# Optimization experiments

Hardware: AMD Instinct MI355X
Metric: run time of the kernel (lower is better)

Reference implementation:

```python
import jax, jax.numpy as jnp
import numpy as np

SCALE = float(np.sqrt(512.0))  # NOTE: module MULTIPLIES by sqrt(dim_attn), not divides


def setup_inputs() -> dict:
    key = jax.random.key(0)
    ks = jax.random.split(key, 10)
    B, N, DQ, DKV, DA = 4, 2048, 512, 512, 512
    w = 0.02  # small init so the *sqrt(d) score scaling stays numerically sane
    return {
        "query": jax.random.normal(ks[0], (B, N, DQ), jnp.float32),
        "key_value": jax.random.normal(ks[1], (B, N, DKV), jnp.float32),
        "Wq": jax.random.normal(ks[2], (DQ, DA), jnp.float32) * w,
        "bq": jnp.zeros((DA,), jnp.float32),
        "Wk": jax.random.normal(ks[3], (DKV, DA), jnp.float32) * w,
        "bk": jnp.zeros((DA,), jnp.float32),
        "Wv": jax.random.normal(ks[4], (DKV, DA), jnp.float32) * w,
        "bv": jnp.zeros((DA,), jnp.float32),
        "Wo": jax.random.normal(ks[5], (DA, DQ), jnp.float32) * w,
        "bo": jnp.zeros((DQ,), jnp.float32),
    }


def reference(query, key_value, Wq, bq, Wk, bk, Wv, bv, Wo, bo):
    # q/k/v projections: (..., dim) @ (dim, dim_attn)
    q = query @ Wq + bq          # [b, nq, da]
    k = key_value @ Wk + bk      # [b, nk, da]
    v = key_value @ Wv + bv      # [b, nk, da]
    # einsum 'dac,dbc->dab' then *sqrt(dim_attn) (faithful: multiply, not divide)
    attn = jnp.einsum('bqc,bkc->bqk', q, k) * SCALE
    attn = jax.nn.softmax(attn, axis=-1)
    # dropout p=0.0 -> no-op
    out = jnp.einsum('bqk,bkc->bqc', attn, v)
    return query + (out @ Wo + bo)
```

## Files before the change

kernel.cpp:

```cpp
#include <hip/hip_runtime.h>

typedef unsigned short u16;
typedef unsigned int u32;
typedef __attribute__((ext_vector_type(8))) __bf16 bf16x8;
typedef __attribute__((ext_vector_type(4))) float f32x4;

#define BK 32

__device__ __forceinline__ u16 f2bf(float x) {
    u32 u = __float_as_uint(x);
    u = (u + 0x7FFFu + ((u >> 16) & 1u)) >> 16;
    return (u16)u;
}
__device__ __forceinline__ float bf2f(u16 h) { return __uint_as_float(((u32)h) << 16); }

#define GLD16(g, l)                                                                        \
    __builtin_amdgcn_global_load_lds((const __attribute__((address_space(1))) void*)(g),   \
                                     (__attribute__((address_space(3))) void*)(l), 16, 0, 0)

template <int N>
__device__ __forceinline__ void vm_wait() {
    if constexpr (N == 0) asm volatile("s_waitcnt vmcnt(0)" ::: "memory");
    else if constexpr (N == 1) asm volatile("s_waitcnt vmcnt(1)" ::: "memory");
    else if constexpr (N == 2) asm volatile("s_waitcnt vmcnt(2)" ::: "memory");
    else if constexpr (N == 3) asm volatile("s_waitcnt vmcnt(3)" ::: "memory");
    else if constexpr (N == 4) asm volatile("s_waitcnt vmcnt(4)" ::: "memory");
    else if constexpr (N == 6) asm volatile("s_waitcnt vmcnt(6)" ::: "memory");
    else if constexpr (N == 8) asm volatile("s_waitcnt vmcnt(8)" ::: "memory");
    else static_assert(N == 0, "unsupported vmcnt literal");
}
#define SBAR() asm volatile("s_barrier" ::: "memory")

__global__ __launch_bounds__(256) void prep_k(
    const float* __restrict__ q, const float* __restrict__ kv,
    u16* __restrict__ QXh, u16* __restrict__ QXl,
    u16* __restrict__ KVh, u16* __restrict__ KVl, long nblk, long n4,
    const float* __restrict__ Wq, const float* __restrict__ Wk,
    const float* __restrict__ Wv, const float* __restrict__ Wo,
    u16* __restrict__ WqTh, u16* __restrict__ WqTl,
    u16* __restrict__ WkvTh, u16* __restrict__ WkvTl,
    u16* __restrict__ WoTh, u16* __restrict__ WoTl, int dim) {
    long b = blockIdx.x;
    if (b < 2 * nblk) {
        const float* x = q; u16* h = QXh; u16* l = QXl;
        if (b >= nblk) { b -= nblk; x = kv; h = KVh; l = KVl; }
        long i = b * 256 + threadIdx.x;
        if (i >= n4) return;
        float4 v = ((const float4*)x)[i];
        float xs[4] = {v.x, v.y, v.z, v.w};
        u16 hh[4], ll[4];
#pragma unroll
        for (int qq = 0; qq < 4; ++qq) {
            hh[qq] = f2bf(xs[qq]);
            ll[qq] = f2bf(xs[qq] - bf2f(hh[qq]));
        }
        uint2 ph, pl;
        ph.x = hh[0] | ((u32)hh[1] << 16); ph.y = hh[2] | ((u32)hh[3] << 16);
        pl.x = ll[0] | ((u32)ll[1] << 16); pl.y = ll[2] | ((u32)ll[3] << 16);
        ((uint2*)h)[i] = ph;
        ((uint2*)l)[i] = pl;
        return;
    }
    long tb = b - 2 * nblk;
    const int z = (int)(tb >> 8);
    const int rem = (int)(tb & 255);
    const long DD = (long)dim * dim;
    const float* W; u16* Th; u16* Tl;
    switch (z) {
        case 0: W = Wq; Th = WqTh; Tl = WqTl; break;
        case 1: W = Wk; Th = WkvTh; Tl = WkvTl; break;
        case 2: W = Wv; Th = WkvTh + DD; Tl = WkvTl + DD; break;
        default: W = Wo; Th = WoTh; Tl = WoTl; break;
    }
    __shared__ float tile[32][33];
    const int bx = (rem & 15) * 32;
    const int by = (rem >> 4) * 32;
    const int tx = threadIdx.x & 31, ty = threadIdx.x >> 5;
    for (int i = 0; i < 32; i += 8)
        tile[ty + i][tx] = W[(size_t)(by + ty + i) * dim + bx + tx];
    __syncthreads();
    for (int i = 0; i < 32; i += 8) {
        float x = tile[tx][ty + i];
        u16 h = f2bf(x);
        size_t idx = (size_t)(bx + ty + i) * dim + by + tx;
        Th[idx] = h;
        Tl[idx] = f2bf(x - bf2f(h));
    }
}

__global__ __launch_bounds__(256) void softmax_k(float* __restrict__ S, int N) {
    float* row = S + (size_t)blockIdx.x * N;
    const int t = threadIdx.x;
    float4 va = ((const float4*)row)[2 * t];
    float4 vb = ((const float4*)row)[2 * t + 1];
    float v[8] = {va.x, va.y, va.z, va.w, vb.x, vb.y, vb.z, vb.w};
    float m = v[0];
#pragma unroll
    for (int i = 1; i < 8; i++) m = fmaxf(m, v[i]);
#pragma unroll
    for (int o = 32; o; o >>= 1) m = fmaxf(m, __shfl_xor(m, o));
    __shared__ float smax[4], ssum[4];
    if ((t & 63) == 0) smax[t >> 6] = m;
    __syncthreads();
    m = fmaxf(fmaxf(smax[0], smax[1]), fmaxf(smax[2], smax[3]));
    float s = 0.f;
#pragma unroll
    for (int i = 0; i < 8; i++) { v[i] = __expf(v[i] - m); s += v[i]; }
#pragma unroll
    for (int o = 32; o; o >>= 1) s += __shfl_xor(s, o);
    if ((t & 63) == 0) ssum[t >> 6] = s;
    __syncthreads();
    s = ssum[0] + ssum[1] + ssum[2] + ssum[3];
    const float inv = 1.0f / s;
    u32 w0 = f2bf(v[0] * inv) | ((u32)f2bf(v[1] * inv) << 16);
    u32 w1 = f2bf(v[2] * inv) | ((u32)f2bf(v[3] * inv) << 16);
    u32 w2 = f2bf(v[4] * inv) | ((u32)f2bf(v[5] * inv) << 16);
    u32 w3 = f2bf(v[6] * inv) | ((u32)f2bf(v[7] * inv) << 16);
    uint4 o4; o4.x = w0; o4.y = w1; o4.z = w2; o4.w = w3;
    ((uint4*)row)[t] = o4;
}

struct GemmArgs {
    const u16 *Ah, *Al; long lda, strideA;
    const u16 *BTh, *BTl; long ldb, strideBT;
    const float *bias1, *bias2; int nsplit;
    const float* resid; long ldres; float scale;
    float* Cf; long ldcf;
    u16 *Cbh, *Cbl; long ldcb;
    u16* CbT; long tRows, tChans, ldct;
    long strideC; int K;
};

template <int SPLIT, int BMt, int BNt>
struct SmemT {
    u16 AsH[2][BMt * BK];
    u16 BsH[2][BNt * BK];
    u16 AsL[2][(SPLIT ? BMt : 1) * BK];
    u16 BsL[2][(SPLIT ? BNt : 1) * BK];
};

template <int SPLIT, int BMt, int BNt, int WR, int WC>
__device__ __forceinline__ void gemm_body(SmemT<SPLIT, BMt, BNt>& sm, const GemmArgs& g,
                                          int bxi, int byi, long bz) {
    static_assert(WR * WC == 4, "4 waves");
    constexpr int MI = BMt / WR / 16;
    constexpr int NJ = BNt / WC / 16;
    constexpr int PA = BMt / 64;
    constexpr int PB = BNt / 64;
    constexpr int NLD = (PA + PB) * (SPLIT ? 2 : 1);

    const u16* Ah = g.Ah + bz * g.strideA;
    const u16* BTh = g.BTh + bz * g.strideBT;
    const u16* Al = nullptr; const u16* BTl = nullptr;
    if constexpr (SPLIT) { Al = g.Al + bz * g.strideA; BTl = g.BTl + bz * g.strideBT; }
    float* Cf = g.Cf ? g.Cf + bz * g.strideC : nullptr;
    u16* Cbh = g.Cbh ? g.Cbh + bz * g.strideC : nullptr;
    u16* Cbl = g.Cbl ? g.Cbl + bz * g.strideC : nullptr;

    const int t = threadIdx.x;
    const int w = t >> 6, lane = t & 63;
    const int l15 = lane & 15, quad = lane >> 4;
    const int m0 = bxi * BMt, n0 = byi * BNt;
    const int wrow = (w / WC) * (BMt / WR);
    const int wcol = (w % WC) * (BNt / WC);

    const u16* gAh[PA]; const u16* gAl[PA]; int lA[PA];
    const u16* gBh[PB]; const u16* gBl[PB]; int lB[PB];
#pragma unroll
    for (int p = 0; p < PA; ++p) {
        int slot = p * 256 + t;
        int r = slot >> 2, c = slot & 3;
        int cg = c ^ ((r >> 1) & 3);
        gAh[p] = Ah + (long)(m0 + r) * g.lda + cg * 8;
        if constexpr (SPLIT) gAl[p] = Al + (long)(m0 + r) * g.lda + cg * 8;
        lA[p] = (p * 256 + w * 64) * 8;
    }
#pragma unroll
    for (int p = 0; p < PB; ++p) {
        int slot = p * 256 + t;
        int r = slot >> 2, c = slot & 3;
        int cg = c ^ ((r >> 1) & 3);
        gBh[p] = BTh + (long)(n0 + r) * g.ldb + cg * 8;
        if constexpr (SPLIT) gBl[p] = BTl + (long)(n0 + r) * g.ldb + cg * 8;
        lB[p] = (p * 256 + w * 64) * 8;
    }

    int aoff[MI], boff[NJ];
#pragma unroll
    for (int i = 0; i < MI; ++i) {
        int r = wrow + i * 16 + l15;
        aoff[i] = (r * 4 + (quad ^ ((r >> 1) & 3))) * 8;
    }
#pragma unroll
    for (int j = 0; j < NJ; ++j) {
        int r = wcol + j * 16 + l15;
        boff[j] = (r * 4 + (quad ^ ((r >> 1) & 3))) * 8;
    }

    f32x4 acc[MI][NJ];
#pragma unroll
    for (int i = 0; i < MI; i++)
#pragma unroll
        for (int j = 0; j < NJ; j++) acc[i][j] = (f32x4){0.f, 0.f, 0.f, 0.f};

    auto stage = [&](int buf) {
#pragma unroll
        for (int p = 0; p < PA; ++p) {
            GLD16(gAh[p], &sm.AsH[buf][lA[p]]);
            gAh[p] += BK;
            if constexpr (SPLIT) { GLD16(gAl[p], &sm.AsL[buf][lA[p]]); gAl[p] += BK; }
        }
#pragma unroll
        for (int p = 0; p < PB; ++p) {
            GLD16(gBh[p], &sm.BsH[buf][lB[p]]);
            gBh[p] += BK;
            if constexpr (SPLIT) { GLD16(gBl[p], &sm.BsL[buf][lB[p]]); gBl[p] += BK; }
        }
    };

    auto compute = [&](int buf) {
        bf16x8 aH[MI], bH[NJ];
#pragma unroll
        for (int i = 0; i < MI; ++i) aH[i] = *(const bf16x8*)&sm.AsH[buf][aoff[i]];
#pragma unroll
        for (int j = 0; j < NJ; ++j) bH[j] = *(const bf16x8*)&sm.BsH[buf][boff[j]];
        if constexpr (SPLIT) {
            bf16x8 aL[MI], bL[NJ];
#pragma unroll
            for (int i = 0; i < MI; ++i) aL[i] = *(const bf16x8*)&sm.AsL[buf][aoff[i]];
#pragma unroll
            for (int j = 0; j < NJ; ++j) bL[j] = *(const bf16x8*)&sm.BsL[buf][boff[j]];
#pragma unroll
            for (int i = 0; i < MI; ++i)
#pragma unroll
                for (int j = 0; j < NJ; ++j) {
                    acc[i][j] = __builtin_amdgcn_mfma_f32_16x16x32_bf16(aH[i], bH[j], acc[i][j], 0, 0, 0);
                    acc[i][j] = __builtin_amdgcn_mfma_f32_16x16x32_bf16(aH[i], bL[j], acc[i][j], 0, 0, 0);
                    acc[i][j] = __builtin_amdgcn_mfma_f32_16x16x32_bf16(aL[i], bH[j], acc[i][j], 0, 0, 0);
                }
        } else {
#pragma unroll
            for (int i = 0; i < MI; ++i)
#pragma unroll
                for (int j = 0; j < NJ; ++j)
                    acc[i][j] = __builtin_amdgcn_mfma_f32_16x16x32_bf16(aH[i], bH[j], acc[i][j], 0, 0, 0);
        }
    };

    const int nt = g.K / BK;
    stage(0);
    if (nt > 1) stage(1);
    for (int tt = 0; tt < nt; tt += 2) {
        if (tt + 1 < nt) vm_wait<NLD>(); else vm_wait<0>();
        SBAR();
        compute(0);
        SBAR();
        if (tt + 2 < nt) stage(0);
        if (tt + 1 < nt) {
            if (tt + 2 < nt) vm_wait<NLD>(); else vm_wait<0>();
            SBAR();
            compute(1);
            SBAR();
            if (tt + 3 < nt) stage(1);
        }
    }

#pragma unroll
    for (int i = 0; i < MI; ++i) {
#pragma unroll
        for (int j = 0; j < NJ; ++j) {
            const int mBase = m0 + wrow + i * 16 + quad * 4;
            const int nn = n0 + wcol + j * 16 + l15;
            const bool norm = nn < g.nsplit;
            float bvs;
            if (norm) bvs = g.bias1 ? g.bias1[nn] : 0.f;
            else bvs = g.bias2 ? g.bias2[nn - g.nsplit] : 0.f;
#pragma unroll
            for (int r = 0; r < 4; ++r) {
                const long row = mBase + r;
                float x = acc[i][j][r] * g.scale + bvs;
                if (g.resid) x += g.resid[row * g.ldres + nn];
                if (norm) {
                    if (Cf) Cf[row * g.ldcf + nn] = x;
                    if (Cbh) {
                        u16 h = f2bf(x);
                        Cbh[row * g.ldcb + nn] = h;
                        if (Cbl) Cbl[row * g.ldcb + nn] = f2bf(x - bf2f(h));
                    }
                } else {
                    long b = row / g.tRows, qq = row - b * g.tRows;
                    g.CbT[(b * g.tChans + (nn - g.nsplit)) * g.ldct + qq] = f2bf(x);
                }
            }
        }
    }
}

template <int SPLIT, int BMt, int BNt, int WR, int WC>
__global__ __launch_bounds__(256) void gemm_k(GemmArgs g) {
    __shared__ SmemT<SPLIT, BMt, BNt> sm;
    gemm_body<SPLIT, BMt, BNt, WR, WC>(sm, g, blockIdx.x, blockIdx.y, blockIdx.z);
}

template <int SPLIT, int BMt, int BNt, int WR, int WC>
__global__ __launch_bounds__(256) void gemm2_k(GemmArgs g0, int ny0, GemmArgs g1) {
    __shared__ SmemT<SPLIT, BMt, BNt> sm;
    if ((int)blockIdx.y < ny0)
        gemm_body<SPLIT, BMt, BNt, WR, WC>(sm, g0, blockIdx.x, blockIdx.y, blockIdx.z);
    else
        gemm_body<SPLIT, BMt, BNt, WR, WC>(sm, g1, blockIdx.x, blockIdx.y - ny0, blockIdx.z);
}

extern "C" void kernel_launch(void* const* d_in, const int* in_sizes, int n_in,
                              void* d_out, int out_size, void* d_ws, size_t ws_size,
                              hipStream_t stream) {
    const float* query = (const float*)d_in[0];
    const float* kv    = (const float*)d_in[1];
    const float* Wq = (const float*)d_in[2];
    const float* bq = (const float*)d_in[3];
    const float* Wk = (const float*)d_in[4];
    const float* bk = (const float*)d_in[5];
    const float* Wv = (const float*)d_in[6];
    const float* bv = (const float*)d_in[7];
    const float* Wo = (const float*)d_in[8];
    const float* bo = (const float*)d_in[9];
    float* out = (float*)d_out;

    const int B = 4, N = 2048, D = 512;
    const long MD = (long)B * N * D;
    const int BIG = 1 << 30;

    char* p = (char*)d_ws;
    auto alloc = [&](size_t bytes) { void* r = (void*)p; p += (bytes + 255) & ~(size_t)255; return r; };
    float* S = (float*)alloc((long)B * N * N * 4);
    u16* QXh = (u16*)S;
    u16* QXl = QXh + MD;
    u16* KVh = QXl + MD;
    u16* KVl = KVh + MD;
    u16* Qh = (u16*)alloc(MD * 2);
    u16* Ql = (u16*)alloc(MD * 2);
    u16* Kh = (u16*)alloc(MD * 2);
    u16* Kl = (u16*)alloc(MD * 2);
    u16* Vt = (u16*)alloc(MD * 2);
    u16* Oh = (u16*)alloc(MD * 2);
    u16* WqTh = (u16*)alloc((long)D * D * 2);
    u16* WqTl = (u16*)alloc((long)D * D * 2);
    u16* WkvTh = (u16*)alloc((long)2 * D * D * 2);
    u16* WkvTl = (u16*)alloc((long)2 * D * D * 2);
    u16* WoTh = (u16*)alloc((long)D * D * 2);
    u16* WoTl = (u16*)alloc((long)D * D * 2);

    const dim3 blk(256, 1, 1);
    const float SCALE = 22.627416997969522f;

    prep_k<<<dim3(2 * 4096 + 1024, 1, 1), blk, 0, stream>>>(
        query, kv, QXh, QXl, KVh, KVl, 4096, MD / 4,
        Wq, Wk, Wv, Wo, WqTh, WqTl, WkvTh, WkvTl, WoTh, WoTl, D);

    GemmArgs qa{};
    qa.Ah = QXh; qa.Al = QXl; qa.lda = D; qa.strideA = 0;
    qa.BTh = WqTh; qa.BTl = WqTl; qa.ldb = D; qa.strideBT = 0;
    qa.bias1 = bq; qa.bias2 = nullptr; qa.nsplit = BIG;
    qa.resid = nullptr; qa.ldres = 0; qa.scale = 1.0f;
    qa.Cf = nullptr; qa.ldcf = 0;
    qa.Cbh = Qh; qa.Cbl = Ql; qa.ldcb = D;
    qa.CbT = nullptr; qa.tRows = 1; qa.tChans = 1; qa.ldct = 1;
    qa.strideC = 0; qa.K = D;

    GemmArgs ka{};
    ka.Ah = KVh; ka.Al = KVl; ka.lda = D; ka.strideA = 0;
    ka.BTh = WkvTh; ka.BTl = WkvTl; ka.ldb = D; ka.strideBT = 0;
    ka.bias1 = bk; ka.bias2 = bv; ka.nsplit = D;
    ka.resid = nullptr; ka.ldres = 0; ka.scale = 1.0f;
    ka.Cf = nullptr; ka.ldcf = 0;
    ka.Cbh = Kh; ka.Cbl = Kl; ka.ldcb = D;
    ka.CbT = Vt; ka.tRows = N; ka.tChans = D; ka.ldct = N;
    ka.strideC = 0; ka.K = D;
    gemm2_k<1, 128, 64, 2, 2><<<dim3(64, 24, 1), blk, 0, stream>>>(qa, 8, ka);

    GemmArgs sa{};
    sa.Ah = Qh; sa.Al = Ql; sa.lda = D; sa.strideA = (long)N * D;
    sa.BTh = Kh; sa.BTl = Kl; sa.ldb = D; sa.strideBT = (long)N * D;
    sa.bias1 = nullptr; sa.bias2 = nullptr; sa.nsplit = BIG;
    sa.resid = nullptr; sa.ldres = 0; sa.scale = SCALE;
    sa.Cf = S; sa.ldcf = N;
    sa.Cbh = nullptr; sa.Cbl = nullptr; sa.ldcb = 0;
    sa.CbT = nullptr; sa.tRows = 1; sa.tChans = 1; sa.ldct = 1;
    sa.strideC = (long)N * N; sa.K = D;
    gemm_k<1, 128, 64, 2, 2><<<dim3(16, 32, 4), blk, 0, stream>>>(sa);

    softmax_k<<<dim3(B * N, 1, 1), blk, 0, stream>>>(S, N);

    GemmArgs pa{};
    pa.Ah = (const u16*)S; pa.Al = nullptr; pa.lda = 2L * N; pa.strideA = (long)N * 2 * N;
    pa.BTh = Vt; pa.BTl = nullptr; pa.ldb = N; pa.strideBT = (long)D * N;
    pa.bias1 = nullptr; pa.bias2 = nullptr; pa.nsplit = BIG;
    pa.resid = nullptr; pa.ldres = 0; pa.scale = 1.0f;
    pa.Cf = nullptr; pa.ldcf = 0;
    pa.Cbh = Oh; pa.Cbl = nullptr; pa.ldcb = D;
    pa.CbT = nullptr; pa.tRows = 1; pa.tChans = 1; pa.ldct = 1;
    pa.strideC = (long)N * D; pa.K = N;
    gemm_k<0, 128, 64, 2, 2><<<dim3(16, 8, 4), blk, 0, stream>>>(pa);

    GemmArgs oa{};
    oa.Ah = Oh; oa.Al = nullptr; oa.lda = D; oa.strideA = 0;
    oa.BTh = WoTh; oa.BTl = nullptr; oa.ldb = D; oa.strideBT = 0;
    oa.bias1 = bo; oa.bias2 = nullptr; oa.nsplit = BIG;
    oa.resid = query; oa.ldres = D; oa.scale = 1.0f;
    oa.Cf = out; oa.ldcf = D;
    oa.Cbh = nullptr; oa.Cbl = nullptr; oa.ldcb = 0;
    oa.CbT = nullptr; oa.tRows = 1; oa.tChans = 1; oa.ldct = 1;
    oa.strideC = 0; oa.K = D;
    gemm_k<0, 128, 64, 2, 2><<<dim3(64, 8, 1), blk, 0, stream>>>(oa);

    (void)in_sizes; (void)n_in; (void)out_size; (void)ws_size;
}
```

Before: 330.4 us.

## Use 8-wave GEMM blocks with per-wave A/B staging split

Switches all GEMM kernels from 4 to 8 waves per 128x64 tile (4x2 wave grid), halving each wave's accumulator footprint. Global-to-LDS staging is reorganised so every wave loads one 16-byte chunk of A, and only the first four waves load B. Per-wave vmcnt waits are adjusted to the differing load counts. The aim is more latency hiding and more MFMA issue parallelism per CU, at the cost of fewer MFMAs per LDS read and more barrier participants.

Result: faster. 279.8 us (-15.3%).

```diff
diff --git a/kernel.cpp b/kernel.cpp
--- a/kernel.cpp
+++ b/kernel.cpp
@@ -142,12 +142,15 @@
 template <int SPLIT, int BMt, int BNt, int WR, int WC>
 __device__ __forceinline__ void gemm_body(SmemT<SPLIT, BMt, BNt>& sm, const GemmArgs& g,
                                           int bxi, int byi, long bz) {
-    static_assert(WR * WC == 4, "4 waves");
+    constexpr int WAVES = WR * WC;
+    static_assert(WAVES == 8, "8-wave kernel");
+    static_assert(BMt / 16 == WAVES, "A staging = 1 GLD16 per wave");
+    constexpr int BW = BNt / 16;
+    static_assert(BW <= WAVES, "");
     constexpr int MI = BMt / WR / 16;
     constexpr int NJ = BNt / WC / 16;
-    constexpr int PA = BMt / 64;
-    constexpr int PB = BNt / 64;
-    constexpr int NLD = (PA + PB) * (SPLIT ? 2 : 1);
+    constexpr int NLD_B = 2 * (SPLIT ? 2 : 1);
+    constexpr int NLD_A = (SPLIT ? 2 : 1);
 
     const u16* Ah = g.Ah + bz * g.strideA;
     const u16* BTh = g.BTh + bz * g.strideBT;
@@ -163,27 +166,24 @@
     const int m0 = bxi * BMt, n0 = byi * BNt;
     const int wrow = (w / WC) * (BMt / WR);
     const int wcol = (w % WC) * (BNt / WC);
-
-    const u16* gAh[PA]; const u16* gAl[PA]; int lA[PA];
-    const u16* gBh[PB]; const u16* gBl[PB]; int lB[PB];
-#pragma unroll
-    for (int p = 0; p < PA; ++p) {
-        int slot = p * 256 + t;
-        int r = slot >> 2, c = slot & 3;
-        int cg = c ^ ((r >> 1) & 3);
-        gAh[p] = Ah + (long)(m0 + r) * g.lda + cg * 8;
-        if constexpr (SPLIT) gAl[p] = Al + (long)(m0 + r) * g.lda + cg * 8;
-        lA[p] = (p * 256 + w * 64) * 8;
-    }
-#pragma unroll
-    for (int p = 0; p < PB; ++p) {
-        int slot = p * 256 + t;
-        int r = slot >> 2, c = slot & 3;
-        int cg = c ^ ((r >> 1) & 3);
-        gBh[p] = BTh + (long)(n0 + r) * g.ldb + cg * 8;
-        if constexpr (SPLIT) gBl[p] = BTl + (long)(n0 + r) * g.ldb + cg * 8;
-        lB[p] = (p * 256 + w * 64) * 8;
-    }
+    const bool hasB = (w < BW);
+
+    {
+    }
+    int uA = w * 64 + lane;
+    int rA = uA >> 2, cA = uA & 3;
+    int cgA = cA ^ ((rA >> 1) & 3);
+    const u16* gAh = Ah + (long)(m0 + rA) * g.lda + cgA * 8;
+    const u16* gAl = nullptr;
+    if constexpr (SPLIT) gAl = Al + (long)(m0 + rA) * g.lda + cgA * 8;
+    const int lA = (w * 64) * 8;
+    int uB = (hasB ? w : 0) * 64 + lane;
+    int rB = uB >> 2, cB = uB & 3;
+    int cgB = cB ^ ((rB >> 1) & 3);
+    const u16* gBh = BTh + (long)(n0 + rB) * g.ldb + cgB * 8;
+    const u16* gBl = nullptr;
+    if constexpr (SPLIT) gBl = BTl + (long)(n0 + rB) * g.ldb + cgB * 8;
+    const int lB = (w * 64) * 8;
 
     int aoff[MI], boff[NJ];
 #pragma unroll
@@ -204,17 +204,13 @@
         for (int j = 0; j < NJ; j++) acc[i][j] = (f32x4){0.f, 0.f, 0.f, 0.f};
 
     auto stage = [&](int buf) {
-#pragma unroll
-        for (int p = 0; p < PA; ++p) {
-            GLD16(gAh[p], &sm.AsH[buf][lA[p]]);
-            gAh[p] += BK;
-            if constexpr (SPLIT) { GLD16(gAl[p], &sm.AsL[buf][lA[p]]); gAl[p] += BK; }
-        }
-#pragma unroll
-        for (int p = 0; p < PB; ++p) {
-            GLD16(gBh[p], &sm.BsH[buf][lB[p]]);
-            gBh[p] += BK;
-            if constexpr (SPLIT) { GLD16(gBl[p], &sm.BsL[buf][lB[p]]); gBl[p] += BK; }
+        GLD16(gAh, &sm.AsH[buf][lA]);
+        gAh += BK;
+        if constexpr (SPLIT) { GLD16(gAl, &sm.AsL[buf][lA]); gAl += BK; }
+        if (hasB) {
+            GLD16(gBh, &sm.BsH[buf][lB]);
+            gBh += BK;
+            if constexpr (SPLIT) { GLD16(gBl, &sm.BsL[buf][lB]); gBl += BK; }
         }
     };
 
@@ -251,13 +247,17 @@
     stage(0);
     if (nt > 1) stage(1);
     for (int tt = 0; tt < nt; tt += 2) {
-        if (tt + 1 < nt) vm_wait<NLD>(); else vm_wait<0>();
+        if (tt + 1 < nt) {
+            if (hasB) vm_wait<NLD_B>(); else vm_wait<NLD_A>();
+        } else vm_wait<0>();
         SBAR();
         compute(0);
         SBAR();
         if (tt + 2 < nt) stage(0);
         if (tt + 1 < nt) {
-            if (tt + 2 < nt) vm_wait<NLD>(); else vm_wait<0>();
+            if (tt + 2 < nt) {
+                if (hasB) vm_wait<NLD_B>(); else vm_wait<NLD_A>();
+            } else vm_wait<0>();
             SBAR();
             compute(1);
             SBAR();
@@ -297,13 +297,13 @@
 }
 
 template <int SPLIT, int BMt, int BNt, int WR, int WC>
-__global__ __launch_bounds__(256) void gemm_k(GemmArgs g) {
+__global__ __launch_bounds__(512) void gemm_k(GemmArgs g) {
     __shared__ SmemT<SPLIT, BMt, BNt> sm;
     gemm_body<SPLIT, BMt, BNt, WR, WC>(sm, g, blockIdx.x, blockIdx.y, blockIdx.z);
 }
 
 template <int SPLIT, int BMt, int BNt, int WR, int WC>
-__global__ __launch_bounds__(256) void gemm2_k(GemmArgs g0, int ny0, GemmArgs g1) {
+__global__ __launch_bounds__(512) void gemm2_k(GemmArgs g0, int ny0, GemmArgs g1) {
     __shared__ SmemT<SPLIT, BMt, BNt> sm;
     if ((int)blockIdx.y < ny0)
         gemm_body<SPLIT, BMt, BNt, WR, WC>(sm, g0, blockIdx.x, blockIdx.y, blockIdx.z);
@@ -351,6 +351,7 @@
     u16* WoTl = (u16*)alloc((long)D * D * 2);
 
     const dim3 blk(256, 1, 1);
+    const dim3 blk8(512, 1, 1);
     const float SCALE = 22.627416997969522f;
 
     prep_k<<<dim3(2 * 4096 + 1024, 1, 1), blk, 0, stream>>>(
@@ -376,7 +377,7 @@
     ka.Cbh = Kh; ka.Cbl = Kl; ka.ldcb = D;
     ka.CbT = Vt; ka.tRows = N; ka.tChans = D; ka.ldct = N;
     ka.strideC = 0; ka.K = D;
-    gemm2_k<1, 128, 64, 2, 2><<<dim3(64, 24, 1), blk, 0, stream>>>(qa, 8, ka);
+    gemm2_k<1, 128, 64, 4, 2><<<dim3(64, 24, 1), blk8, 0, stream>>>(qa, 8, ka);
 
     GemmArgs sa{};
     sa.Ah = Qh; sa.Al = Ql; sa.lda = D; sa.strideA = (long)N * D;
@@ -387,7 +388,7 @@
     sa.Cbh = nullptr; sa.Cbl = nullptr; sa.ldcb = 0;
     sa.CbT = nullptr; sa.tRows = 1; sa.tChans = 1; sa.ldct = 1;
     sa.strideC = (long)N * N; sa.K = D;
-    gemm_k<1, 128, 64, 2, 2><<<dim3(16, 32, 4), blk, 0, stream>>>(sa);
+    gemm_k<1, 128, 64, 4, 2><<<dim3(16, 32, 4), blk8, 0, stream>>>(sa);
 
     softmax_k<<<dim3(B * N, 1, 1), blk, 0, stream>>>(S, N);
 
@@ -400,7 +401,7 @@
     pa.Cbh = Oh; pa.Cbl = nullptr; pa.ldcb = D;
     pa.CbT = nullptr; pa.tRows = 1; pa.tChans = 1; pa.ldct = 1;
     pa.strideC = (long)N * D; pa.K = N;
-    gemm_k<0, 128, 64, 2, 2><<<dim3(16, 8, 4), blk, 0, stream>>>(pa);
+    gemm_k<0, 128, 64, 4, 2><<<dim3(16, 8, 4), blk8, 0, stream>>>(pa);
 
     GemmArgs oa{};
     oa.Ah = Oh; oa.Al = nullptr; oa.lda = D; oa.strideA = 0;
@@ -411,7 +412,7 @@
     oa.Cbh = nullptr; oa.Cbl = nullptr; oa.ldcb = 0;
     oa.CbT = nullptr; oa.tRows = 1; oa.tChans = 1; oa.ldct = 1;
     oa.strideC = 0; oa.K = D;
-    gemm_k<0, 128, 64, 2, 2><<<dim3(64, 8, 1), blk, 0, stream>>>(oa);
+    gemm_k<0, 128, 64, 4, 2><<<dim3(64, 8, 1), blk8, 0, stream>>>(oa);
 
     (void)in_sizes; (void)n_in; (void)out_size; (void)ws_size;
 }
```
